# Optimization experiments

Hardware: AMD Instinct MI355X
Metric: run time of the kernel (lower is better)

The kernel has to match this reference:

```python
import jax, jax.numpy as jnp
import numpy as np

N_HEADS = 16
D_KV = 64
NUM_BUCKETS = 64      # bidirectional T5 buckets
MAX_DISTANCE = 50     # hist_step


def _rel_bucket(rel_pos):
    # T5 bidirectional relative-position bucketing.
    nb = NUM_BUCKETS // 2
    ret = (rel_pos > 0).astype(jnp.int32) * nb
    n = jnp.abs(rel_pos)
    max_exact = nb // 2
    is_small = n < max_exact
    large = max_exact + (
        jnp.log(jnp.maximum(n, 1).astype(jnp.float32) / max_exact)
        / np.log(MAX_DISTANCE / max_exact)
        * (nb - max_exact)
    ).astype(jnp.int32)
    large = jnp.minimum(large, nb - 1)
    return ret + jnp.where(is_small, n, large)


def _position_bias(rel_table, qlen, klen):
    ctx = jnp.arange(qlen)[:, None]
    mem = jnp.arange(klen)[None, :]
    bucket = _rel_bucket(mem - ctx)            # (q, k)
    vals = rel_table[bucket]                   # (q, k, h)
    return jnp.transpose(vals, (2, 0, 1))[None]  # (1, h, q, k)


def setup_inputs() -> dict:
    key = jax.random.key(0)
    ks = jax.random.split(key, 11)
    bs, qlen, d_model = 2, 2048, 1024
    inner = N_HEADS * D_KV
    s = 0.02
    return {
        "x": jax.random.normal(ks[0], (bs, qlen, d_model), jnp.float32),
        "Wq": jax.random.normal(ks[1], (d_model, inner), jnp.float32) * s,
        "bq": jnp.zeros((inner,), jnp.float32),
        "Wk": jax.random.normal(ks[2], (d_model, inner), jnp.float32) * s,
        "bk": jnp.zeros((inner,), jnp.float32),
        "Wv": jax.random.normal(ks[3], (d_model, inner), jnp.float32) * s,
        "bv": jnp.zeros((inner,), jnp.float32),
        "Wo": jax.random.normal(ks[4], (inner, d_model), jnp.float32) * s,
        "bo": jnp.zeros((d_model,), jnp.float32),
        "rel_table": jax.random.normal(ks[5], (NUM_BUCKETS, N_HEADS), jnp.float32) * s,
        "mask": jax.random.randint(ks[6], (bs, qlen), 0, 2) > 0,
    }


def reference(x, Wq, bq, Wk, bk, Wv, bv, Wo, bo, rel_table, mask):
    bs, qlen, d_model = x.shape

    def shape(h):  # (b, s, inner) -> (b, n, s, d)
        return h.reshape(bs, qlen, N_HEADS, D_KV).transpose(0, 2, 1, 3)

    q = shape(x @ Wq + bq)
    k = shape(x @ Wk + bk)
    v = shape(x @ Wv + bv)

    # No 1/sqrt(d) scaling in T5.
    scores = jnp.einsum('bnqd,bnkd->bnqk', q, k)

    mask_f = jnp.where(mask, -jnp.inf, 0.0).astype(scores.dtype)[:, None, None, :]  # (b,1,1,k)
    pos_bias = _position_bias(rel_table, qlen, qlen)  # (1,h,q,k)
    add = pos_bias + mask_f                           # bias + mask, broadcast over q

    weights = jax.nn.softmax(scores + add, axis=-1)   # dropout p=0 -> identity
    context = jnp.einsum('bnqk,bnkd->bnqd', weights, v)
    context = context.transpose(0, 2, 1, 3).reshape(bs, qlen, N_HEADS * D_KV)
    out = context @ Wo + bo
    return out, weights, pos_bias
```

## Files before the change

### kernel.cpp

```cpp
#include <hip/hip_runtime.h>
#include <math.h>

typedef _Float16 f16;
typedef f16 f16x8 __attribute__((ext_vector_type(8)));
typedef f16 f16x4 __attribute__((ext_vector_type(4)));
typedef float f32x4 __attribute__((ext_vector_type(4)));

#define W_OFF   (2*2048*1024)
#define PB_OFF  (W_OFF + 2LL*16*2048*2048)

#define NEG_BIG (-1.0e30f)

__device__ __forceinline__ void gload_lds16(const f16* g, f16* l) {
    __builtin_amdgcn_global_load_lds(
        (const __attribute__((address_space(1))) void*)g,
        (__attribute__((address_space(3))) void*)l,
        16, 0, 0);
}

__device__ __forceinline__ int rel_bucket(int rel) {
    int ret = rel > 0 ? 32 : 0;
    int n = rel < 0 ? -rel : rel;
    if (n < 16) return ret + n;
    float fn = (float)n;
    float t = logf(fn * (1.0f / 16.0f));
    t = t / 1.1394343f;
    int large = 16 + (int)(t * 16.0f);
    if (large > 31) large = 31;
    return ret + large;
}


__global__ __launch_bounds__(256)
void conv_f16_kernel(const float* __restrict__ in, f16* __restrict__ out) {
    size_t i = ((size_t)blockIdx.x * 256 + threadIdx.x) * 4;
    float4 v = *(const float4*)&in[i];
    f16x4 h = { (f16)v.x, (f16)v.y, (f16)v.z, (f16)v.w };
    *(f16x4*)&out[i] = h;
}

__global__ __launch_bounds__(256)
void transpose_w_kernel(const float* __restrict__ W, f16* __restrict__ Wt) {
    __shared__ float tile[64 * 68];
    const int tid = threadIdx.x;
    const int bi = blockIdx.x, bj = blockIdx.y;
    #pragma unroll
    for (int it = 0; it < 4; ++it) {
        int slot = tid + it * 256;
        int row = slot >> 4, col4 = (slot & 15) * 4;
        float4 v = *(const float4*)&W[(size_t)(bi * 64 + row) * 1024 + bj * 64 + col4];
        *(float4*)&tile[row * 68 + col4] = v;
    }
    __syncthreads();
    #pragma unroll
    for (int it = 0; it < 4; ++it) {
        int slot = tid + it * 256;
        int nrow = slot >> 4, kcol4 = (slot & 15) * 4;
        f16x4 h;
        #pragma unroll
        for (int j = 0; j < 4; ++j)
            h[j] = (f16)tile[(kcol4 + j) * 68 + nrow];
        *(f16x4*)&Wt[(size_t)(bj * 64 + nrow) * 1024 + bi * 64 + kcol4] = h;
    }
}

__global__ __launch_bounds__(256)
void bias_tbl_kernel(const float* __restrict__ rel_table, float* __restrict__ tbl) {
    int idx = blockIdx.x * 256 + threadIdx.x;
    int h = idx >> 12, dd = idx & 4095;
    tbl[idx] = rel_table[rel_bucket(dd - 2047) * 16 + h];
}

__global__ __launch_bounds__(256)
void concat_bias_kernel(const float* __restrict__ bq, const float* __restrict__ bk,
                        const float* __restrict__ bv, float* __restrict__ o) {
    int i = blockIdx.x * 256 + threadIdx.x;
    float v = i < 1024 ? bq[i] : (i < 2048 ? bk[i - 1024] : bv[i - 2048]);
    o[i] = v;
}

__global__ __launch_bounds__(256)
void transpose_v_kernel(const f16* __restrict__ vh, f16* __restrict__ vt) {
    __shared__ f16 tile[64 * 72];
    const int tid = threadIdx.x;
    const int st = blockIdx.x, bh = blockIdx.y;
    #pragma unroll
    for (int it = 0; it < 2; ++it) {
        int slot = tid + it * 256;
        int row = slot >> 3, col8 = (slot & 7) * 8;
        f16x8 v = *(const f16x8*)&vh[((size_t)bh * 2048 + st * 64 + row) * 64 + col8];
        *(f16x8*)&tile[row * 72 + col8] = v;
    }
    __syncthreads();
    #pragma unroll
    for (int it = 0; it < 2; ++it) {
        int slot = tid + it * 256;
        int drow = slot >> 3, scol8 = (slot & 7) * 8;
        f16x8 r;
        #pragma unroll
        for (int j = 0; j < 8; ++j)
            r[j] = tile[(scol8 + j) * 72 + drow];
        *(f16x8*)&vt[((size_t)bh * 64 + drow) * 2048 + st * 64 + scol8] = r;
    }
}

__global__ __launch_bounds__(256)
void gemm_f16(const f16* __restrict__ A, const f16* __restrict__ Bt,
              const float* __restrict__ bias, void* __restrict__ Cout, int mode)
{
    __shared__ f16 aLDS[128 * 32];
    __shared__ f16 bLDS[128 * 32];
    const int tid = threadIdx.x;
    const int lane = tid & 63, wv = tid >> 6;
    const int quad = lane >> 4, l15 = lane & 15;
    const int wm = (wv & 1) * 64, wn = (wv >> 1) * 64;
    const int bm = blockIdx.y * 128, bn = blockIdx.x * 128;

    f32x4 acc[4][4];
    #pragma unroll
    for (int i = 0; i < 4; ++i)
        #pragma unroll
        for (int j = 0; j < 4; ++j)
            acc[i][j] = (f32x4){0.f, 0.f, 0.f, 0.f};

    for (int k0 = 0; k0 < 1024; k0 += 32) {
        __syncthreads();
        #pragma unroll
        for (int s = 0; s < 2; ++s) {
            int row = (wv + s * 4) * 16 + l15;
            gload_lds16(&A [(size_t)(bm + row) * 1024 + k0 + quad * 8],
                        &aLDS[(size_t)(s * 256 + wv * 64) * 8]);
            gload_lds16(&Bt[(size_t)(bn + row) * 1024 + k0 + quad * 8],
                        &bLDS[(size_t)(s * 256 + wv * 64) * 8]);
        }
        __syncthreads();
        f16x8 af[4], bf[4];
        #pragma unroll
        for (int i = 0; i < 4; ++i) {
            af[i] = *(const f16x8*)&aLDS[(((wm >> 4) + i) * 64 + lane) * 8];
            bf[i] = *(const f16x8*)&bLDS[(((wn >> 4) + i) * 64 + lane) * 8];
        }
        #pragma unroll
        for (int i = 0; i < 4; ++i)
            #pragma unroll
            for (int j = 0; j < 4; ++j)
                acc[i][j] = __builtin_amdgcn_mfma_f32_16x16x32_f16(af[i], bf[j], acc[i][j], 0, 0, 0);
    }

    #pragma unroll
    for (int j = 0; j < 4; ++j) {
        int n = bn + wn + j * 16 + l15;
        float bz = bias[n];
        #pragma unroll
        for (int i = 0; i < 4; ++i) {
            #pragma unroll
            for (int r = 0; r < 4; ++r) {
                int m = bm + wm + i * 16 + quad * 4 + r;
                float val = acc[i][j][r] + bz;
                if (mode == 0) {
                    ((float*)Cout)[(size_t)m * 1024 + n] = val;
                } else {
                    int b = m >> 11, srow = m & 2047;
                    int buf = n >> 10, h = (n >> 6) & 15, d = n & 63;
                    ((f16*)Cout)[(size_t)buf * 4194304 +
                                 (((size_t)(b * 16 + h) * 2048 + srow) << 6) + d] = (f16)val;
                }
            }
        }
    }
}

__global__ __launch_bounds__(256)
void attn_f16(const f16* __restrict__ qh, const f16* __restrict__ kh,
              const f16* __restrict__ vth, const float* __restrict__ tbl,
              const int* __restrict__ mask, float* __restrict__ wout,
              f16* __restrict__ ctxh)
{
    __shared__ float biasL[4096];
    __shared__ float maskL[2048];
    __shared__ f16 kL[8 * 64 * 8];
    __shared__ f16 vL[8 * 64 * 8];
    __shared__ f16 wnat[4 * 16 * 88];

    const int tid = threadIdx.x, lane = tid & 63, wv = tid >> 6;
    const int quad = lane >> 4, l15 = lane & 15;

    const int lin = blockIdx.y * 32 + blockIdx.x;
    const int nl = (lin & 7) * 128 + (lin >> 3);
    const int bh = nl >> 5, b = bh >> 4, h = bh & 15;
    const int qt0 = (nl & 31) * 64;

    for (int i = tid; i < 1024; i += 256)
        *(float4*)&biasL[i * 4] = *(const float4*)&tbl[h * 4096 + i * 4];
    for (int i = tid; i < 512; i += 256) {
        int4 mv = *(const int4*)&mask[b * 2048 + i * 4];
        float4 f;
        f.x = mv.x ? NEG_BIG : -20.f;  f.y = mv.y ? NEG_BIG : -20.f;
        f.z = mv.z ? NEG_BIG : -20.f;  f.w = mv.w ? NEG_BIG : -20.f;
        *(float4*)&maskL[i * 4] = f;
    }

    const int q0 = qt0 + wv * 16;
    f16x8 aq[2];
    #pragma unroll
    for (int ds = 0; ds < 2; ++ds)
        aq[ds] = *(const f16x8*)&qh[((size_t)bh * 2048 + q0 + l15) * 64 + ds * 32 + quad * 8];

    const int qrow_base = q0 + quad * 4;
    const f16* kB = kh  + (size_t)bh * 2048 * 64;
    const f16* vB = vth + (size_t)bh * 64 * 2048;

    float lI[4] = {0.f, 0.f, 0.f, 0.f};

    for (int c = 0; c < 32; ++c) {
        __syncthreads();
        #pragma unroll
        for (int s = 0; s < 2; ++s) {
            int f = wv + s * 4;
            int dstep = f >> 2, nt = f & 3;
            gload_lds16(&kB[(size_t)(c * 64 + nt * 16 + l15) * 64 + dstep * 32 + quad * 8],
                        &kL[(size_t)(s * 256 + wv * 64) * 8]);
        }
        __syncthreads();
        #pragma unroll
        for (int nt = 0; nt < 4; ++nt) {
            f32x4 s4 = (f32x4){0.f, 0.f, 0.f, 0.f};
            #pragma unroll
            for (int ds = 0; ds < 2; ++ds) {
                f16x8 bf = *(const f16x8*)&kL[((ds * 4 + nt) * 64 + lane) * 8];
                s4 = __builtin_amdgcn_mfma_f32_16x16x32_f16(aq[ds], bf, s4, 0, 0, 0);
            }
            int k = c * 64 + nt * 16 + l15;
            float mk = maskL[k];
            int bi = k - qrow_base + 2047;
            #pragma unroll
            for (int r = 0; r < 4; ++r)
                lI[r] += __expf(s4[r] + biasL[bi - r] + mk);
        }
    }
    #pragma unroll
    for (int r = 0; r < 4; ++r) {
        float l = lI[r];
        l += __shfl_xor(l, 1, 64);
        l += __shfl_xor(l, 2, 64);
        l += __shfl_xor(l, 4, 64);
        l += __shfl_xor(l, 8, 64);
        lI[r] = 1.0f / l;
    }

    float* wbase = wout + (size_t)bh * 2048 * 2048;
    f32x4 oacc[4];
    #pragma unroll
    for (int nt = 0; nt < 4; ++nt) oacc[nt] = (f32x4){0.f, 0.f, 0.f, 0.f};

    for (int c = 0; c < 32; ++c) {
        __syncthreads();
        #pragma unroll
        for (int s = 0; s < 2; ++s) {
            int f = wv + s * 4;
            {
                int dstep = f >> 2, nt = f & 3;
                gload_lds16(&kB[(size_t)(c * 64 + nt * 16 + l15) * 64 + dstep * 32 + quad * 8],
                            &kL[(size_t)(s * 256 + wv * 64) * 8]);
            }
            {
                int ks = f >> 2, nt = f & 3;
                gload_lds16(&vB[(size_t)(nt * 16 + l15) * 2048 + c * 64 + ks * 32 + quad * 8],
                            &vL[(size_t)(s * 256 + wv * 64) * 8]);
            }
        }
        __syncthreads();

        #pragma unroll
        for (int nt = 0; nt < 4; ++nt) {
            f32x4 s4 = (f32x4){0.f, 0.f, 0.f, 0.f};
            #pragma unroll
            for (int ds = 0; ds < 2; ++ds) {
                f16x8 bf = *(const f16x8*)&kL[((ds * 4 + nt) * 64 + lane) * 8];
                s4 = __builtin_amdgcn_mfma_f32_16x16x32_f16(aq[ds], bf, s4, 0, 0, 0);
            }
            int k = c * 64 + nt * 16 + l15;
            float mk = maskL[k];
            int bi = k - qrow_base + 2047;
            float* wp = wbase + (size_t)qrow_base * 2048 + k;
            #pragma unroll
            for (int r = 0; r < 4; ++r) {
                float w = __expf(s4[r] + biasL[bi - r] + mk) * lI[r];
                wp[(size_t)r * 2048] = w;
                wnat[wv * 1408 + (quad * 4 + r) * 88 + nt * 16 + l15] = (f16)w;
            }
        }
        #pragma unroll
        for (int ks = 0; ks < 2; ++ks) {
            f16x8 wf = *(const f16x8*)&wnat[wv * 1408 + l15 * 88 + ks * 32 + quad * 8];
            #pragma unroll
            for (int nt = 0; nt < 4; ++nt) {
                f16x8 vf = *(const f16x8*)&vL[((ks * 4 + nt) * 64 + lane) * 8];
                oacc[nt] = __builtin_amdgcn_mfma_f32_16x16x32_f16(wf, vf, oacc[nt], 0, 0, 0);
            }
        }
    }

    #pragma unroll
    for (int nt = 0; nt < 4; ++nt) {
        int d = nt * 16 + l15;
        #pragma unroll
        for (int r = 0; r < 4; ++r) {
            int q = qrow_base + r;
            ctxh[((size_t)(b * 2048) + q) * 1024 + h * 64 + d] = (f16)oacc[nt][r];
        }
    }
}

__global__ __launch_bounds__(256)
void posbias_kernel(const float* __restrict__ rel_table, float* __restrict__ pb)
{
    size_t g = ((size_t)blockIdx.x * 256 + threadIdx.x) * 4;
    int k = (int)(g & 2047);
    int q = (int)((g >> 11) & 2047);
    int h = (int)(g >> 22);
    float4 r;
    float* rp = (float*)&r;
    #pragma unroll
    for (int j = 0; j < 4; ++j)
        rp[j] = rel_table[rel_bucket(k + j - q) * 16 + h];
    *(float4*)&pb[g] = r;
}

__global__ __launch_bounds__(256)
void posbias_tbl_kernel(const float* __restrict__ tblw, float* __restrict__ pb)
{
    size_t g = ((size_t)blockIdx.x * 256 + threadIdx.x) * 4;
    int k = (int)(g & 2047);
    int q = (int)((g >> 11) & 2047);
    int h = (int)(g >> 22);
    const float* tp = tblw + h * 4096 + (k - q + 2047);
    float4 r = { tp[0], tp[1], tp[2], tp[3] };
    *(float4*)&pb[g] = r;
}

extern "C" void kernel_launch(void* const* d_in, const int* in_sizes, int n_in,
                              void* d_out, int out_size, void* d_ws, size_t ws_size,
                              hipStream_t stream) {
    const float* x    = (const float*)d_in[0];
    const float* Wq   = (const float*)d_in[1];
    const float* bq   = (const float*)d_in[2];
    const float* Wk   = (const float*)d_in[3];
    const float* bk   = (const float*)d_in[4];
    const float* Wv   = (const float*)d_in[5];
    const float* bv   = (const float*)d_in[6];
    const float* Wo   = (const float*)d_in[7];
    const float* bo   = (const float*)d_in[8];
    const float* rt   = (const float*)d_in[9];
    const int*   mask = (const int*)d_in[10];

    float* out = (float*)d_out;
    float* wts = out + W_OFF;
    float* pb  = out + PB_OFF;

    float* tbl  = pb;
    f16*   xh   = (f16*)(pb + 65536);
    f16*   wqt  = (f16*)(pb + 2162688);
    f16*   wkt  = (f16*)(pb + 2686976);
    f16*   wvt  = (f16*)(pb + 3211264);
    f16*   wot  = (f16*)(pb + 3735552);
    f16*   qh   = (f16*)(pb + 4259840);
    f16*   kh   = (f16*)(pb + 6356992);
    f16*   vh   = (f16*)(pb + 8454144);
    f16*   vth  = (f16*)(pb + 10551296);
    f16*   ctxh = (f16*)(pb + 12648448);
    float* bqkv = pb + 14745600;

    const bool use_ws = ws_size >= 65536 * sizeof(float);
    float* tblw = (float*)d_ws;

    dim3 blk(256);
    conv_f16_kernel<<<dim3(4096), blk, 0, stream>>>(x, xh);
    transpose_w_kernel<<<dim3(16, 16), blk, 0, stream>>>(Wq, wqt);
    transpose_w_kernel<<<dim3(16, 16), blk, 0, stream>>>(Wk, wkt);
    transpose_w_kernel<<<dim3(16, 16), blk, 0, stream>>>(Wv, wvt);
    transpose_w_kernel<<<dim3(16, 16), blk, 0, stream>>>(Wo, wot);
    bias_tbl_kernel<<<dim3(256), blk, 0, stream>>>(rt, tbl);
    if (use_ws)
        bias_tbl_kernel<<<dim3(256), blk, 0, stream>>>(rt, tblw);
    concat_bias_kernel<<<dim3(12), blk, 0, stream>>>(bq, bk, bv, bqkv);

    gemm_f16<<<dim3(24, 32), blk, 0, stream>>>(xh, wqt, bqkv, qh, 1);
    transpose_v_kernel<<<dim3(32, 32), blk, 0, stream>>>(vh, vth);

    attn_f16<<<dim3(32, 32), blk, 0, stream>>>(qh, kh, vth, tbl, mask, wts, ctxh);

    gemm_f16<<<dim3(8, 32), blk, 0, stream>>>(ctxh, wot, bo, out, 0);

    if (use_ws)
        posbias_tbl_kernel<<<dim3(65536), blk, 0, stream>>>(tblw, pb);
    else
        posbias_kernel<<<dim3(65536), blk, 0, stream>>>(rt, pb);
}
```

Baseline: 1.115 ms.

## Fuse prep kernels, widen attention blocks, emit position bias from attention

```diff
diff --git a/kernel.cpp b/kernel.cpp
--- a/kernel.cpp
+++ b/kernel.cpp
@@ -30,20 +30,43 @@
     return ret + large;
 }
 
-
-__global__ __launch_bounds__(256)
-void conv_f16_kernel(const float* __restrict__ in, f16* __restrict__ out) {
-    size_t i = ((size_t)blockIdx.x * 256 + threadIdx.x) * 4;
-    float4 v = *(const float4*)&in[i];
-    f16x4 h = { (f16)v.x, (f16)v.y, (f16)v.z, (f16)v.w };
-    *(f16x4*)&out[i] = h;
-}
-
-__global__ __launch_bounds__(256)
-void transpose_w_kernel(const float* __restrict__ W, f16* __restrict__ Wt) {
+__global__ __launch_bounds__(256)
+void prep_misc_kernel(const float* __restrict__ x, f16* __restrict__ xh,
+                      const float* __restrict__ rt, float* __restrict__ tbl,
+                      float* __restrict__ tblw,
+                      const float* __restrict__ bq, const float* __restrict__ bk,
+                      const float* __restrict__ bv, float* __restrict__ bqkv)
+{
+    const int bid = blockIdx.x, tid = threadIdx.x;
+    if (bid < 4096) {
+        size_t i = ((size_t)bid * 256 + tid) * 4;
+        float4 v = *(const float4*)&x[i];
+        f16x4 h = { (f16)v.x, (f16)v.y, (f16)v.z, (f16)v.w };
+        *(f16x4*)&xh[i] = h;
+    } else if (bid < 4352) {
+        int idx = (bid - 4096) * 256 + tid;
+        int h = idx >> 12, dd = idx & 4095;
+        tbl[idx] = rt[rel_bucket(dd - 2047) * 16 + h];
+    } else if (bid < 4608) {
+        int idx = (bid - 4352) * 256 + tid;
+        int h = idx >> 12, dd = idx & 4095;
+        tblw[idx] = rt[rel_bucket(dd - 2047) * 16 + h];
+    } else {
+        int i = (bid - 4608) * 256 + tid;
+        float v = i < 1024 ? bq[i] : (i < 2048 ? bk[i - 1024] : bv[i - 2048]);
+        bqkv[i] = v;
+    }
+}
+
+__global__ __launch_bounds__(256)
+void transpose_w4_kernel(const float* __restrict__ Wq, const float* __restrict__ Wk,
+                         const float* __restrict__ Wv, const float* __restrict__ Wo,
+                         f16* __restrict__ WtBase) {
     __shared__ float tile[64 * 68];
     const int tid = threadIdx.x;
-    const int bi = blockIdx.x, bj = blockIdx.y;
+    const int bi = blockIdx.x, bj = blockIdx.y, z = blockIdx.z;
+    const float* W = z == 0 ? Wq : z == 1 ? Wk : z == 2 ? Wv : Wo;
+    f16* Wt = WtBase + (size_t)z * 1048576;
     #pragma unroll
     for (int it = 0; it < 4; ++it) {
         int slot = tid + it * 256;
@@ -62,21 +85,6 @@
             h[j] = (f16)tile[(kcol4 + j) * 68 + nrow];
         *(f16x4*)&Wt[(size_t)(bj * 64 + nrow) * 1024 + bi * 64 + kcol4] = h;
     }
-}
-
-__global__ __launch_bounds__(256)
-void bias_tbl_kernel(const float* __restrict__ rel_table, float* __restrict__ tbl) {
-    int idx = blockIdx.x * 256 + threadIdx.x;
-    int h = idx >> 12, dd = idx & 4095;
-    tbl[idx] = rel_table[rel_bucket(dd - 2047) * 16 + h];
-}
-
-__global__ __launch_bounds__(256)
-void concat_bias_kernel(const float* __restrict__ bq, const float* __restrict__ bk,
-                        const float* __restrict__ bv, float* __restrict__ o) {
-    int i = blockIdx.x * 256 + threadIdx.x;
-    float v = i < 1024 ? bq[i] : (i < 2048 ? bk[i - 1024] : bv[i - 2048]);
-    o[i] = v;
 }
 
 __global__ __launch_bounds__(256)
@@ -170,34 +178,39 @@
     }
 }
 
-__global__ __launch_bounds__(256)
+__global__ __launch_bounds__(512, 4)
 void attn_f16(const f16* __restrict__ qh, const f16* __restrict__ kh,
               const f16* __restrict__ vth, const float* __restrict__ tbl,
               const int* __restrict__ mask, float* __restrict__ wout,
-              f16* __restrict__ ctxh)
+              f16* __restrict__ ctxh, float* __restrict__ pbout)
 {
-    __shared__ float biasL[4096];
-    __shared__ float maskL[2048];
+    __shared__ f16 biasH[4096];
+    __shared__ f16 maskH[2048];
     __shared__ f16 kL[8 * 64 * 8];
     __shared__ f16 vL[8 * 64 * 8];
-    __shared__ f16 wnat[4 * 16 * 88];
+    __shared__ f16 wnat[8 * 16 * 88];
 
     const int tid = threadIdx.x, lane = tid & 63, wv = tid >> 6;
     const int quad = lane >> 4, l15 = lane & 15;
 
-    const int lin = blockIdx.y * 32 + blockIdx.x;
-    const int nl = (lin & 7) * 128 + (lin >> 3);
-    const int bh = nl >> 5, b = bh >> 4, h = bh & 15;
-    const int qt0 = (nl & 31) * 64;
-
-    for (int i = tid; i < 1024; i += 256)
-        *(float4*)&biasL[i * 4] = *(const float4*)&tbl[h * 4096 + i * 4];
-    for (int i = tid; i < 512; i += 256) {
+    const int lin = blockIdx.x;
+    const int nl = (lin & 7) * 64 + (lin >> 3);
+    const int bh = nl >> 4, b = bh >> 4, h = bh & 15;
+    const int qt0 = (nl & 15) * 128;
+
+    for (int i = tid; i < 1024; i += 512) {
+        float4 v = *(const float4*)&tbl[h * 4096 + i * 4];
+        f16x4 hh = { (f16)v.x, (f16)v.y, (f16)v.z, (f16)v.w };
+        *(f16x4*)&biasH[i * 4] = hh;
+    }
+    for (int i = tid; i < 512; i += 512) {
         int4 mv = *(const int4*)&mask[b * 2048 + i * 4];
-        float4 f;
-        f.x = mv.x ? NEG_BIG : -20.f;  f.y = mv.y ? NEG_BIG : -20.f;
-        f.z = mv.z ? NEG_BIG : -20.f;  f.w = mv.w ? NEG_BIG : -20.f;
-        *(float4*)&maskL[i * 4] = f;
+        f16x4 f;
+        f.x = mv.x ? (f16)(-60000.f) : (f16)(-20.f);
+        f.y = mv.y ? (f16)(-60000.f) : (f16)(-20.f);
+        f.z = mv.z ? (f16)(-60000.f) : (f16)(-20.f);
+        f.w = mv.w ? (f16)(-60000.f) : (f16)(-20.f);
+        *(f16x4*)&maskH[i * 4] = f;
     }
 
     const int q0 = qt0 + wv * 16;
@@ -209,18 +222,14 @@
     const int qrow_base = q0 + quad * 4;
     const f16* kB = kh  + (size_t)bh * 2048 * 64;
     const f16* vB = vth + (size_t)bh * 64 * 2048;
+    const int fnt = wv & 3, fds = wv >> 2;
 
     float lI[4] = {0.f, 0.f, 0.f, 0.f};
 
     for (int c = 0; c < 32; ++c) {
         __syncthreads();
-        #pragma unroll
-        for (int s = 0; s < 2; ++s) {
-            int f = wv + s * 4;
-            int dstep = f >> 2, nt = f & 3;
-            gload_lds16(&kB[(size_t)(c * 64 + nt * 16 + l15) * 64 + dstep * 32 + quad * 8],
-                        &kL[(size_t)(s * 256 + wv * 64) * 8]);
-        }
+        gload_lds16(&kB[(size_t)(c * 64 + fnt * 16 + l15) * 64 + fds * 32 + quad * 8],
+                    &kL[(size_t)(wv * 64) * 8]);
         __syncthreads();
         #pragma unroll
         for (int nt = 0; nt < 4; ++nt) {
@@ -231,11 +240,11 @@
                 s4 = __builtin_amdgcn_mfma_f32_16x16x32_f16(aq[ds], bf, s4, 0, 0, 0);
             }
             int k = c * 64 + nt * 16 + l15;
-            float mk = maskL[k];
+            float mk = (float)maskH[k];
             int bi = k - qrow_base + 2047;
             #pragma unroll
             for (int r = 0; r < 4; ++r)
-                lI[r] += __expf(s4[r] + biasL[bi - r] + mk);
+                lI[r] += __expf(s4[r] + (float)biasH[bi - r] + mk);
         }
     }
     #pragma unroll
@@ -249,26 +258,17 @@
     }
 
     float* wbase = wout + (size_t)bh * 2048 * 2048;
+    float* pbh = (pbout && b == 0) ? pbout + (size_t)h * 2048 * 2048 : (float*)0;
     f32x4 oacc[4];
     #pragma unroll
     for (int nt = 0; nt < 4; ++nt) oacc[nt] = (f32x4){0.f, 0.f, 0.f, 0.f};
 
     for (int c = 0; c < 32; ++c) {
         __syncthreads();
-        #pragma unroll
-        for (int s = 0; s < 2; ++s) {
-            int f = wv + s * 4;
-            {
-                int dstep = f >> 2, nt = f & 3;
-                gload_lds16(&kB[(size_t)(c * 64 + nt * 16 + l15) * 64 + dstep * 32 + quad * 8],
-                            &kL[(size_t)(s * 256 + wv * 64) * 8]);
-            }
-            {
-                int ks = f >> 2, nt = f & 3;
-                gload_lds16(&vB[(size_t)(nt * 16 + l15) * 2048 + c * 64 + ks * 32 + quad * 8],
-                            &vL[(size_t)(s * 256 + wv * 64) * 8]);
-            }
-        }
+        gload_lds16(&kB[(size_t)(c * 64 + fnt * 16 + l15) * 64 + fds * 32 + quad * 8],
+                    &kL[(size_t)(wv * 64) * 8]);
+        gload_lds16(&vB[(size_t)(fnt * 16 + l15) * 2048 + c * 64 + fds * 32 + quad * 8],
+                    &vL[(size_t)(wv * 64) * 8]);
         __syncthreads();
 
         #pragma unroll
@@ -280,14 +280,17 @@
                 s4 = __builtin_amdgcn_mfma_f32_16x16x32_f16(aq[ds], bf, s4, 0, 0, 0);
             }
             int k = c * 64 + nt * 16 + l15;
-            float mk = maskL[k];
+            float mk = (float)maskH[k];
             int bi = k - qrow_base + 2047;
             float* wp = wbase + (size_t)qrow_base * 2048 + k;
             #pragma unroll
             for (int r = 0; r < 4; ++r) {
-                float w = __expf(s4[r] + biasL[bi - r] + mk) * lI[r];
+                float bz = (float)biasH[bi - r];
+                float w = __expf(s4[r] + bz + mk) * lI[r];
                 wp[(size_t)r * 2048] = w;
                 wnat[wv * 1408 + (quad * 4 + r) * 88 + nt * 16 + l15] = (f16)w;
+                if (pbh)
+                    pbh[(size_t)(qrow_base + r) * 2048 + k] = bz;
             }
         }
         #pragma unroll
@@ -358,42 +361,40 @@
     float* wts = out + W_OFF;
     float* pb  = out + PB_OFF;
 
-    float* tbl  = pb;
-    f16*   xh   = (f16*)(pb + 65536);
-    f16*   wqt  = (f16*)(pb + 2162688);
-    f16*   wkt  = (f16*)(pb + 2686976);
-    f16*   wvt  = (f16*)(pb + 3211264);
-    f16*   wot  = (f16*)(pb + 3735552);
-    f16*   qh   = (f16*)(pb + 4259840);
-    f16*   kh   = (f16*)(pb + 6356992);
-    f16*   vh   = (f16*)(pb + 8454144);
-    f16*   vth  = (f16*)(pb + 10551296);
-    f16*   ctxh = (f16*)(pb + 12648448);
-    float* bqkv = pb + 14745600;
-
-    const bool use_ws = ws_size >= 65536 * sizeof(float);
-    float* tblw = (float*)d_ws;
+    const size_t SCRATCH_FLOATS = 14748672ULL;
+    const bool ws_full  = ws_size >= SCRATCH_FLOATS * 4;
+    const bool ws_small = ws_size >= 65536 * 4;
+
+    float* base = ws_full ? (float*)d_ws : pb;
+
+    float* tbl  = base;
+    f16*   xh   = (f16*)(base + 65536);
+    f16*   wqt  = (f16*)(base + 2162688);
+    f16*   qh   = (f16*)(base + 4259840);
+    f16*   kh   = (f16*)(base + 6356992);
+    f16*   vh   = (f16*)(base + 8454144);
+    f16*   vth  = (f16*)(base + 10551296);
+    f16*   ctxh = (f16*)(base + 12648448);
+    float* bqkv = base + 14745600;
+
+    float* tblw = ws_full ? tbl : (ws_small ? (float*)d_ws : tbl);
 
     dim3 blk(256);
-    conv_f16_kernel<<<dim3(4096), blk, 0, stream>>>(x, xh);
-    transpose_w_kernel<<<dim3(16, 16), blk, 0, stream>>>(Wq, wqt);
-    transpose_w_kernel<<<dim3(16, 16), blk, 0, stream>>>(Wk, wkt);
-    transpose_w_kernel<<<dim3(16, 16), blk, 0, stream>>>(Wv, wvt);
-    transpose_w_kernel<<<dim3(16, 16), blk, 0, stream>>>(Wo, wot);
-    bias_tbl_kernel<<<dim3(256), blk, 0, stream>>>(rt, tbl);
-    if (use_ws)
-        bias_tbl_kernel<<<dim3(256), blk, 0, stream>>>(rt, tblw);
-    concat_bias_kernel<<<dim3(12), blk, 0, stream>>>(bq, bk, bv, bqkv);
+    prep_misc_kernel<<<dim3(4620), blk, 0, stream>>>(x, xh, rt, tbl, tblw, bq, bk, bv, bqkv);
+    transpose_w4_kernel<<<dim3(16, 16, 4), blk, 0, stream>>>(Wq, Wk, Wv, Wo, wqt);
 
     gemm_f16<<<dim3(24, 32), blk, 0, stream>>>(xh, wqt, bqkv, qh, 1);
     transpose_v_kernel<<<dim3(32, 32), blk, 0, stream>>>(vh, vth);
 
-    attn_f16<<<dim3(32, 32), blk, 0, stream>>>(qh, kh, vth, tbl, mask, wts, ctxh);
-
-    gemm_f16<<<dim3(8, 32), blk, 0, stream>>>(ctxh, wot, bo, out, 0);
-
-    if (use_ws)
-        posbias_tbl_kernel<<<dim3(65536), blk, 0, stream>>>(tblw, pb);
-    else
-        posbias_kernel<<<dim3(65536), blk, 0, stream>>>(rt, pb);
-}
+    attn_f16<<<dim3(512), dim3(512), 0, stream>>>(qh, kh, vth, tbl, mask, wts, ctxh,
+                                                  ws_full ? pb : (float*)0);
+
+    gemm_f16<<<dim3(8, 32), blk, 0, stream>>>(ctxh, wqt + 3 * 1048576, bo, out, 0);
+
+    if (!ws_full) {
+        if (ws_small)
+            posbias_tbl_kernel<<<dim3(65536), blk, 0, stream>>>(tblw, pb);
+        else
+            posbias_kernel<<<dim3(65536), blk, 0, stream>>>(rt, pb);
+    }
+}
```

Measured after the change: 1.140 ms. +2.3%, slower.
